# Kernel tuning notes

Hardware: AMD Instinct MI355X
Metric: run time of the kernel (lower is better)

Reference implementation:

```python
import jax, jax.numpy as jnp
import numpy as np

NH, NP, MA, FL = 8, 4, 2, 3   # heads, points, max_num_agent, feature_level
L = MA * FL                    # total sampling levels = 6
C = 256
BS, NQ = 8, 4096
SS = np.array([[64, 64], [32, 32], [16, 16]] * MA, dtype=np.int64)  # [L,2] (H,W)
NV = int((SS[:, 0] * SS[:, 1]).sum())  # 10752


def setup_inputs() -> dict:
    key = jax.random.key(0)
    ks = jax.random.split(key, 8)
    f32 = jnp.float32
    return {
        'query': jax.random.normal(ks[0], (BS, NQ, C), f32),
        'query_pos': jax.random.normal(ks[1], (BS, NQ, C), f32),
        'value': jax.random.normal(ks[2], (BS, NV, C), f32),
        'reference_points': jax.random.uniform(ks[3], (BS, NQ, L, 2), f32),
        'spatial_shapes': SS,
        'W_off': jax.random.normal(ks[4], (C, L * NH * NP * 2), f32) * 0.01,
        'b_off': jnp.zeros((L * NH * NP * 2,), f32),
        'W_attn': jax.random.normal(ks[5], (C, L * NH * NP), f32) * 0.05,
        'b_attn': jnp.zeros((L * NH * NP,), f32),
        'W_val': jax.random.normal(ks[6], (C, C), f32) * 0.05,
        'b_val': jnp.zeros((C,), f32),
        'W_out': jax.random.normal(ks[7], (C, C), f32) * 0.05,
        'b_out': jnp.zeros((C,), f32),
    }


def _ms_deform_attn(v, loc, attn, ss):
    # v: [bs, nv, NH, d]; loc: [bs, nq, NH, L, NP, 2] in [0,1] (x,y)
    # attn: [bs, nq, NH, L, NP]; ss: np int array [L,2] (H,W) -- static
    bs, nq = loc.shape[0], loc.shape[1]
    d = v.shape[-1]
    starts = np.concatenate([[0], np.cumsum(ss[:, 0] * ss[:, 1])[:-1]])
    out = jnp.zeros((bs, NH, nq, d), v.dtype)
    for l in range(L):
        H, W = int(ss[l, 0]), int(ss[l, 1])
        s0 = int(starts[l])
        vl = v[:, s0:s0 + H * W].transpose(0, 2, 1, 3)  # [bs, NH, HW, d]
        # sampling coords, grid_sample align_corners=False convention
        x = loc[:, :, :, l, :, 0].transpose(0, 2, 1, 3) * W - 0.5  # [bs,NH,nq,NP]
        y = loc[:, :, :, l, :, 1].transpose(0, 2, 1, 3) * H - 0.5
        x0 = jnp.floor(x); y0 = jnp.floor(y)
        lx = x - x0; ly = y - y0
        x0i = x0.astype(jnp.int32); y0i = y0.astype(jnp.int32)

        def gather(yi, xi):
            valid = (yi >= 0) & (yi < H) & (xi >= 0) & (xi < W)
            idx = jnp.clip(yi, 0, H - 1) * W + jnp.clip(xi, 0, W - 1)  # [bs,NH,nq,NP]
            g = jnp.take_along_axis(vl, idx.reshape(bs, NH, nq * NP, 1), axis=2)
            g = g.reshape(bs, NH, nq, NP, d)
            return g * valid[..., None].astype(g.dtype)  # zero padding outside

        sampled = ((1 - lx) * (1 - ly))[..., None] * gather(y0i, x0i) \
                + (lx * (1 - ly))[..., None] * gather(y0i, x0i + 1) \
                + ((1 - lx) * ly)[..., None] * gather(y0i + 1, x0i) \
                + (lx * ly)[..., None] * gather(y0i + 1, x0i + 1)
        aw = attn[:, :, :, l, :].transpose(0, 2, 1, 3)  # [bs,NH,nq,NP]
        out = out + jnp.einsum('bhqpd,bhqp->bhqd', sampled, aw)
    return out.transpose(0, 2, 1, 3).reshape(bs, nq, NH * d)


def reference(query, query_pos, value, reference_points, spatial_shapes,
              W_off, b_off, W_attn, b_attn, W_val, b_val, W_out, b_out):
    ss = np.asarray(spatial_shapes)
    identity = query
    q = query + query_pos
    bs, nv, c = value.shape
    nq = q.shape[1]
    v = (value @ W_val + b_val).reshape(bs, nv, NH, c // NH)
    off = (q @ W_off + b_off).reshape(bs, nq, NH, L, NP, 2)
    attn = (q @ W_attn + b_attn).reshape(bs, nq, NH, L * NP)
    attn = jax.nn.softmax(attn, axis=-1).reshape(bs, nq, NH, L, NP)
    offset_normalizer = jnp.asarray(np.stack([ss[:, 1], ss[:, 0]], -1), q.dtype)  # [L,2] (W,H)
    loc = reference_points[:, :, None, :, None, :] \
        + off / offset_normalizer[None, None, None, :, None, :]
    out = _ms_deform_attn(v, loc, attn, ss)
    out = out @ W_out + b_out
    return out + identity  # dropout is identity in eval mode
```

## Files before the change

kernel.cpp:

```cpp
#include <hip/hip_runtime.h>

#define NHEAD 8
#define NPOINT 4
#define NLVL 6
#define CDIM 256
#define BSZ 8
#define NQRY 4096
#define NVAL 10752

typedef __attribute__((ext_vector_type(8))) short short8;
typedef __attribute__((ext_vector_type(4))) float floatx4;
typedef __attribute__((ext_vector_type(2))) float float2v;

__device__ __forceinline__ unsigned short f2bf(float f) {
    unsigned u = __float_as_uint(f);
    return (unsigned short)((u + 0x7FFFu + ((u >> 16) & 1u)) >> 16);
}
__device__ __forceinline__ unsigned pack2(float a, float b) {
    return (unsigned)f2bf(a) | ((unsigned)f2bf(b) << 16);
}
__device__ __forceinline__ float blo(unsigned u) { return __uint_as_float(u << 16); }
__device__ __forceinline__ float bhi(unsigned u) { return __uint_as_float(u & 0xffff0000u); }

__global__ __launch_bounds__(256) void prep_w(
    const float* __restrict__ Wv, const float* __restrict__ Woff,
    const float* __restrict__ Wattn, const float* __restrict__ Wo,
    unsigned short* __restrict__ Wt)
{
    const int id = blockIdx.x * 256 + threadIdx.x;
    const int n = id >> 8, k = id & 255;
    float val;
    if (n < 256) val = Wv[k * 256 + n];
    else if (n < 832) {
        const int nn = n - 256;
        val = (nn < 384) ? Woff[k * 384 + nn] : Wattn[k * 192 + (nn - 384)];
    } else val = Wo[k * 256 + (n - 832)];
    Wt[id] = f2bf(val);
}

__global__ __launch_bounds__(256) void q_conv(
    const float* __restrict__ query, const float* __restrict__ qpos,
    unsigned short* __restrict__ qbf)
{
    const long i = ((long)blockIdx.x * 256 + threadIdx.x) * 4;
    const float4 a = *(const float4*)(query + i);
    const float4 b = *(const float4*)(qpos + i);
    ushort4 r;
    r.x = f2bf(a.x + b.x); r.y = f2bf(a.y + b.y);
    r.z = f2bf(a.z + b.z); r.w = f2bf(a.w + b.w);
    *(ushort4*)(qbf + i) = r;
}

template<int BN, int ABF, int VTRANS, int RESID, int SPLITB>
__global__ __launch_bounds__(512) void gemm_mfma(
    const void* __restrict__ Av, const unsigned short* __restrict__ Bt,
    const float* __restrict__ bias, const float* __restrict__ bias2,
    const float* __restrict__ resid, void* __restrict__ Cv,
    int M, int Ntot)
{
    constexpr int BK = 32, BMt = 128, PAD = 8;
    constexpr int WN = BN / 4, NT = WN / 16;
    __shared__ unsigned short As[BMt][BK + PAD];
    __shared__ unsigned short Bs[BN][BK + PAD];
    const int tid = threadIdx.x;
    const int bm = blockIdx.y * BMt;
    const int bcol = blockIdx.x * BN;
    const int wid = tid >> 6, lane = tid & 63;
    const int wm = (wid >> 2) * 64, wn = (wid & 3) * WN;
    const int lm = lane & 15, q8 = (lane >> 4) * 8;

    floatx4 acc[4][NT];
#pragma unroll
    for (int i = 0; i < 4; ++i)
#pragma unroll
        for (int j = 0; j < NT; ++j) acc[i][j] = (floatx4)0.0f;

    const int arow = tid >> 2, akp = (tid & 3) * 8;
    const int bn_ = tid >> 1, bkp = (tid & 1) * 16;

    for (int k0 = 0; k0 < 256; k0 += BK) {
        if (ABF) {
            const unsigned short* A = (const unsigned short*)Av;
            uint4 v = *(const uint4*)(A + (long)(bm + arow) * 256 + k0 + akp);
            *(uint4*)&As[arow][akp] = v;
        } else {
            const float* A = (const float*)Av;
            const float* p = A + (long)(bm + arow) * 256 + k0 + akp;
            const float4 a = *(const float4*)p;
            const float4 b = *(const float4*)(p + 4);
            uint4 v;
            v.x = pack2(a.x, a.y); v.y = pack2(a.z, a.w);
            v.z = pack2(b.x, b.y); v.w = pack2(b.z, b.w);
            *(uint4*)&As[arow][akp] = v;
        }
        if (bn_ < BN) {
            const unsigned short* p = Bt + (long)(bcol + bn_) * 256 + k0 + bkp;
            uint4 v0 = *(const uint4*)p;
            uint4 v1 = *(const uint4*)(p + 8);
            *(uint4*)&Bs[bn_][bkp] = v0;
            *(uint4*)&Bs[bn_][bkp + 8] = v1;
        }
        __syncthreads();
        short8 af[4], bfr[NT];
#pragma unroll
        for (int i = 0; i < 4; ++i) af[i] = *(const short8*)&As[wm + i * 16 + lm][q8];
#pragma unroll
        for (int j = 0; j < NT; ++j) bfr[j] = *(const short8*)&Bs[wn + j * 16 + lm][q8];
#pragma unroll
        for (int i = 0; i < 4; ++i)
#pragma unroll
            for (int j = 0; j < NT; ++j)
                acc[i][j] = __builtin_amdgcn_mfma_f32_16x16x32_bf16(af[i], bfr[j], acc[i][j], 0, 0, 0);
        __syncthreads();
    }

    const int qrow = (lane >> 4) * 4;
#pragma unroll
    for (int j = 0; j < NT; ++j) {
        const int colg = bcol + wn + j * 16 + lm;
        const float bv = (SPLITB && colg >= 384) ? bias2[colg - 384] : bias[colg];
#pragma unroll
        for (int i = 0; i < 4; ++i) {
#pragma unroll
            for (int r = 0; r < 4; ++r) {
                const int rowl = wm + i * 16 + qrow + r;
                const int rowg = bm + rowl;
                float val = acc[i][j][r] + bv;
                if (VTRANS) {
                    const int b = bm / NVAL;
                    const int pos = bm - b * NVAL + rowl;
                    const int h = colg >> 5, d = colg & 31;
                    ((unsigned short*)Cv)[(((long)(b * NHEAD + h)) * NVAL + pos) * 32 + d] = f2bf(val);
                } else {
                    if (RESID) val += resid[(long)rowg * 256 + colg];
                    ((float*)Cv)[(long)rowg * Ntot + colg] = val;
                }
            }
        }
    }
}

__global__ __launch_bounds__(256) void ms_sample4(
    const unsigned short* __restrict__ v,
    const float* __restrict__ oa,
    const float* __restrict__ refp,
    unsigned short* __restrict__ outi)
{
    __shared__ float s_rec[4][192 * 6];
    __shared__ float s_ref[4][12];
    const int tid = threadIdx.x;
    const int w = tid >> 6;
    const int lane = tid & 63;
    const int bq = blockIdx.x * 4 + w;
    const int b = bq >> 12;

    if (lane < 12) s_ref[w][lane] = refp[(long)bq * 12 + lane];
    __syncthreads();

    const int h = lane >> 3;
    const int li = lane & 7;
    const float* oarow = oa + (long)bq * 576;

    const float* lgp = oarow + 384 + h * 24 + li * 3;
    const float lg0 = lgp[0], lg1 = lgp[1], lg2 = lgp[2];
    float mx = fmaxf(lg0, fmaxf(lg1, lg2));
    mx = fmaxf(mx, __shfl_xor(mx, 1));
    mx = fmaxf(mx, __shfl_xor(mx, 2));
    mx = fmaxf(mx, __shfl_xor(mx, 4));
    const float e0 = __expf(lg0 - mx);
    const float e1 = __expf(lg1 - mx);
    const float e2 = __expf(lg2 - mx);
    float den = e0 + e1 + e2;
    den += __shfl_xor(den, 1);
    den += __shfl_xor(den, 2);
    den += __shfl_xor(den, 4);
    const float inv = 1.0f / den;
    const float aw_[3] = {e0 * inv, e1 * inv, e2 * inv};

    const float* offp = oarow + (h * 24 + li * 3) * 2;
    const float2v od0 = *(const float2v*)(offp);
    const float2v od1 = *(const float2v*)(offp + 2);
    const float2v od2 = *(const float2v*)(offp + 4);

#pragma unroll
    for (int k = 0; k < 3; ++k) {
        const int lp = li * 3 + k;
        const int l = lp >> 2;
        const int sh = (l >= 3) ? (l - 3) : l;
        const int W = 64 >> sh;
        const int base = ((l >= 3) ? 5376 : 0)
                       + ((sh >= 1) ? 4096 : 0)
                       + ((sh >= 2) ? 1024 : 0);
        const float Wf = (float)W;
        const float ox = (k == 0) ? od0.x : (k == 1) ? od1.x : od2.x;
        const float oy = (k == 0) ? od0.y : (k == 1) ? od1.y : od2.y;
        const float rx = s_ref[w][l * 2 + 0];
        const float ry = s_ref[w][l * 2 + 1];
        const float x = rx * Wf + ox - 0.5f;
        const float y = ry * Wf + oy - 0.5f;
        const float xf = floorf(x), yf = floorf(y);
        const int x0 = (int)xf, y0 = (int)yf;
        const float lx = x - xf, ly = y - yf;
        const float wx0 = (x0 >= 0 && x0 < W)      ? (1.f - lx) : 0.f;
        const float wx1 = (x0 >= -1 && x0 < W - 1) ? lx         : 0.f;
        const float wy0 = (y0 >= 0 && y0 < W)      ? (1.f - ly) : 0.f;
        const float wy1 = (y0 >= -1 && y0 < W - 1) ? ly         : 0.f;
        const int x0c = min(max(x0, 0), W - 1);
        const int x1c = min(max(x0 + 1, 0), W - 1);
        const int y0c = min(max(y0, 0), W - 1);
        const int y1c = min(max(y0 + 1, 0), W - 1);
        const float aw = aw_[k];
        const unsigned p00 = (unsigned)(base + y0c * W + x0c);
        const unsigned p01 = (unsigned)(base + y0c * W + x1c);
        const unsigned p10 = (unsigned)(base + y1c * W + x0c);
        const unsigned p11 = (unsigned)(base + y1c * W + x1c);
        float* r = &s_rec[w][((lp << 3) + h) * 6];
        float2v wa, wb;
        wa.x = aw * wx0 * wy0; wa.y = aw * wx1 * wy0;
        wb.x = aw * wx0 * wy1; wb.y = aw * wx1 * wy1;
        *(float2v*)(r)     = wa;
        *(float2v*)(r + 2) = wb;
        uint2 pk;
        pk.x = p00 | (p01 << 16);
        pk.y = p10 | (p11 << 16);
        *(uint2*)(r + 4) = pk;
    }
    __syncthreads();

    const unsigned short* vb = v + ((long)(b * NHEAD + h)) * NVAL * 32 + li * 4;
    float2v acc01 = {0.f, 0.f};
    float2v acc23 = {0.f, 0.f};
    const float* rp0 = &s_rec[w][h * 6];

#pragma unroll 4
    for (int lp = 0; lp < NLVL * NPOINT; ++lp) {
        const float* rp = rp0 + lp * 48;
        const float2v w01 = *(const float2v*)(rp);
        const float2v w23 = *(const float2v*)(rp + 2);
        const uint2 pp = *(const uint2*)(rp + 4);
        const uint2 u00 = *(const uint2*)(vb + ((pp.x & 0xffffu) << 5));
        const uint2 u01 = *(const uint2*)(vb + ((pp.x >> 16) << 5));
        const uint2 u10 = *(const uint2*)(vb + ((pp.y & 0xffffu) << 5));
        const uint2 u11 = *(const uint2*)(vb + ((pp.y >> 16) << 5));
        float2v c;
        c.x = blo(u00.x); c.y = bhi(u00.x); acc01 += w01.x * c;
        c.x = blo(u00.y); c.y = bhi(u00.y); acc23 += w01.x * c;
        c.x = blo(u01.x); c.y = bhi(u01.x); acc01 += w01.y * c;
        c.x = blo(u01.y); c.y = bhi(u01.y); acc23 += w01.y * c;
        c.x = blo(u10.x); c.y = bhi(u10.x); acc01 += w23.x * c;
        c.x = blo(u10.y); c.y = bhi(u10.y); acc23 += w23.x * c;
        c.x = blo(u11.x); c.y = bhi(u11.x); acc01 += w23.y * c;
        c.x = blo(u11.y); c.y = bhi(u11.y); acc23 += w23.y * c;
    }
    ushort4 o;
    o.x = f2bf(acc01.x); o.y = f2bf(acc01.y);
    o.z = f2bf(acc23.x); o.w = f2bf(acc23.y);
    *(ushort4*)(outi + (long)bq * CDIM + lane * 4) = o;
}

extern "C" void kernel_launch(void* const* d_in, const int* in_sizes, int n_in,
                              void* d_out, int out_size, void* d_ws, size_t ws_size,
                              hipStream_t stream) {
    const float* query     = (const float*)d_in[0];
    const float* query_pos = (const float*)d_in[1];
    const float* value     = (const float*)d_in[2];
    const float* refp      = (const float*)d_in[3];
    const float* W_off  = (const float*)d_in[5];
    const float* b_off  = (const float*)d_in[6];
    const float* W_attn = (const float*)d_in[7];
    const float* b_attn = (const float*)d_in[8];
    const float* W_val  = (const float*)d_in[9];
    const float* b_val  = (const float*)d_in[10];
    const float* W_out  = (const float*)d_in[11];
    const float* b_out  = (const float*)d_in[12];
    float* out = (float*)d_out;

    unsigned short* v_bf = (unsigned short*)d_ws;
    unsigned short* q_bf = v_bf + (long)86016 * 256;
    unsigned short* Wt   = q_bf + (long)32768 * 256;
    float* oa_ws = (float*)(Wt + (long)1088 * 256);
    unsigned short* i_bf = (unsigned short*)(oa_ws + (long)32768 * 576);

    const int MV = BSZ * NVAL;
    const int MQ = BSZ * NQRY;

    prep_w<<<1088, 256, 0, stream>>>(W_val, W_off, W_attn, W_out, Wt);
    q_conv<<<(MQ * CDIM / 4) / 256, 256, 0, stream>>>(query, query_pos, q_bf);
    gemm_mfma<256, 0, 1, 0, 0><<<dim3(1, MV / 128), 512, 0, stream>>>(
        value, Wt, b_val, nullptr, nullptr, v_bf, MV, 256);
    gemm_mfma<192, 1, 0, 0, 1><<<dim3(3, MQ / 128), 512, 0, stream>>>(
        q_bf, Wt + (long)256 * 256, b_off, b_attn, nullptr, oa_ws, MQ, 576);
    ms_sample4<<<MQ / 4, 256, 0, stream>>>(v_bf, oa_ws, refp, i_bf);
    gemm_mfma<256, 1, 0, 1, 0><<<dim3(1, MQ / 128), 512, 0, stream>>>(
        i_bf, Wt + (long)832 * 256, b_out, nullptr, query, out, MQ, 256);
}
```

Measured before the change: 399.0 us.

## Fetch horizontally adjacent bilinear corners with one 16-byte load per row

The sampling kernel now clamps the left corner to W-2 so that the two horizontal neighbours are contiguous in memory. It folds the x-weights into a left/right choice so each lane issues one 16-byte load per row instead of two 8-byte loads per corner pair. Lanes split the work by left/right corner and combine partial sums with a cross-lane shuffle before writing bf16 output. This halves the number of gather instructions, at the cost of extra weight-selection logic, a shuffle reduction, and byte offsets held in 32-bit indices.

```diff
diff --git a/kernel.cpp b/kernel.cpp
--- a/kernel.cpp
+++ b/kernel.cpp
@@ -205,57 +205,66 @@
         const float wx1 = (x0 >= -1 && x0 < W - 1) ? lx         : 0.f;
         const float wy0 = (y0 >= 0 && y0 < W)      ? (1.f - ly) : 0.f;
         const float wy1 = (y0 >= -1 && y0 < W - 1) ? ly         : 0.f;
-        const int x0c = min(max(x0, 0), W - 1);
-        const int x1c = min(max(x0 + 1, 0), W - 1);
         const int y0c = min(max(y0, 0), W - 1);
         const int y1c = min(max(y0 + 1, 0), W - 1);
+        const int xb = min(max(x0, 0), W - 2);
+        const float wl = (xb == x0) ? wx0 : ((xb == x0 + 1) ? wx1 : 0.f);
+        const float wr = (xb == x0) ? wx1 : ((xb == x0 - 1) ? wx0 : 0.f);
         const float aw = aw_[k];
-        const unsigned p00 = (unsigned)(base + y0c * W + x0c);
-        const unsigned p01 = (unsigned)(base + y0c * W + x1c);
-        const unsigned p10 = (unsigned)(base + y1c * W + x0c);
-        const unsigned p11 = (unsigned)(base + y1c * W + x1c);
+        const float awl = aw * wl, awr = aw * wr;
         float* r = &s_rec[w][((lp << 3) + h) * 6];
-        float2v wa, wb;
-        wa.x = aw * wx0 * wy0; wa.y = aw * wx1 * wy0;
-        wb.x = aw * wx0 * wy1; wb.y = aw * wx1 * wy1;
-        *(float2v*)(r)     = wa;
-        *(float2v*)(r + 2) = wb;
+        float2v wlv, wrv;
+        wlv.x = awl * wy0; wlv.y = awl * wy1;
+        wrv.x = awr * wy0; wrv.y = awr * wy1;
+        *(float2v*)(r)     = wlv;
+        *(float2v*)(r + 2) = wrv;
         uint2 pk;
-        pk.x = p00 | (p01 << 16);
-        pk.y = p10 | (p11 << 16);
+        pk.x = (unsigned)(base + y0c * W + xb) * 64u;
+        pk.y = (unsigned)(base + y1c * W + xb) * 64u;
         *(uint2*)(r + 4) = pk;
     }
     __syncthreads();
 
-    const unsigned short* vb = v + ((long)(b * NHEAD + h)) * NVAL * 32 + li * 4;
-    float2v acc01 = {0.f, 0.f};
-    float2v acc23 = {0.f, 0.f};
+    const unsigned lane_base =
+        (unsigned)((b * NHEAD + h) * NVAL) * 64u + (unsigned)li * 16u;
+    const char* vbase = (const char*)v;
+    const int sel = (li >> 2) * 2;
     const float* rp0 = &s_rec[w][h * 6];
-
-#pragma unroll 4
+    float2v a01 = {0.f, 0.f}, a23 = {0.f, 0.f};
+    float2v a45 = {0.f, 0.f}, a67 = {0.f, 0.f};
+
+#pragma unroll 8
     for (int lp = 0; lp < NLVL * NPOINT; ++lp) {
         const float* rp = rp0 + lp * 48;
-        const float2v w01 = *(const float2v*)(rp);
-        const float2v w23 = *(const float2v*)(rp + 2);
-        const uint2 pp = *(const uint2*)(rp + 4);
-        const uint2 u00 = *(const uint2*)(vb + ((pp.x & 0xffffu) << 5));
-        const uint2 u01 = *(const uint2*)(vb + ((pp.x >> 16) << 5));
-        const uint2 u10 = *(const uint2*)(vb + ((pp.y & 0xffffu) << 5));
-        const uint2 u11 = *(const uint2*)(vb + ((pp.y >> 16) << 5));
+        const float2v wv = *(const float2v*)(rp + sel);
+        const uint2 off = *(const uint2*)(rp + 4);
+        const uint4 u0 = *(const uint4*)(vbase + (lane_base + off.x));
+        const uint4 u1 = *(const uint4*)(vbase + (lane_base + off.y));
         float2v c;
-        c.x = blo(u00.x); c.y = bhi(u00.x); acc01 += w01.x * c;
-        c.x = blo(u00.y); c.y = bhi(u00.y); acc23 += w01.x * c;
-        c.x = blo(u01.x); c.y = bhi(u01.x); acc01 += w01.y * c;
-        c.x = blo(u01.y); c.y = bhi(u01.y); acc23 += w01.y * c;
-        c.x = blo(u10.x); c.y = bhi(u10.x); acc01 += w23.x * c;
-        c.x = blo(u10.y); c.y = bhi(u10.y); acc23 += w23.x * c;
-        c.x = blo(u11.x); c.y = bhi(u11.x); acc01 += w23.y * c;
-        c.x = blo(u11.y); c.y = bhi(u11.y); acc23 += w23.y * c;
+        c.x = blo(u0.x); c.y = bhi(u0.x); a01 += wv.x * c;
+        c.x = blo(u0.y); c.y = bhi(u0.y); a23 += wv.x * c;
+        c.x = blo(u0.z); c.y = bhi(u0.z); a45 += wv.x * c;
+        c.x = blo(u0.w); c.y = bhi(u0.w); a67 += wv.x * c;
+        c.x = blo(u1.x); c.y = bhi(u1.x); a01 += wv.y * c;
+        c.x = blo(u1.y); c.y = bhi(u1.y); a23 += wv.y * c;
+        c.x = blo(u1.z); c.y = bhi(u1.z); a45 += wv.y * c;
+        c.x = blo(u1.w); c.y = bhi(u1.w); a67 += wv.y * c;
     }
+
+    a01.x += __shfl_xor(a01.x, 4); a01.y += __shfl_xor(a01.y, 4);
+    a23.x += __shfl_xor(a23.x, 4); a23.y += __shfl_xor(a23.y, 4);
+    a45.x += __shfl_xor(a45.x, 4); a45.y += __shfl_xor(a45.y, 4);
+    a67.x += __shfl_xor(a67.x, 4); a67.y += __shfl_xor(a67.y, 4);
+
+    const int hi = li >> 2;
+    const float o0 = hi ? a45.x : a01.x;
+    const float o1 = hi ? a45.y : a01.y;
+    const float o2 = hi ? a67.x : a23.x;
+    const float o3 = hi ? a67.y : a23.y;
     ushort4 o;
-    o.x = f2bf(acc01.x); o.y = f2bf(acc01.y);
-    o.z = f2bf(acc23.x); o.w = f2bf(acc23.y);
-    *(ushort4*)(outi + (long)bq * CDIM + lane * 4) = o;
+    o.x = f2bf(o0); o.y = f2bf(o1); o.z = f2bf(o2); o.w = f2bf(o3);
+    const int d = (li & 3) * 8 + hi * 4;
+    *(ushort4*)(outi + (long)bq * CDIM + h * 32 + d) = o;
 }
 
 extern "C" void kernel_launch(void* const* d_in, const int* in_sizes, int n_in,
```

After: 394.0 us. About the same (-1.2%).
